# Optimization experiments

Hardware: AMD Instinct MI355X
Metric: run time of the kernel (lower is better)

Reference implementation:

```python
import jax, jax.numpy as jnp
import numpy as np

B, C, H, W = 64, 512, 8, 8
K = 100            # num_class
H1, HID, L = 64, 128, 32   # ae_hidden[0], fixed hidd, ae_latent
CLIP = 100.0       # CSSRClassifier.clip_len
RED = -0.1         # model='pcssr' -> -1, times gamma=0.1
PUSH_THRESH = 10000.0


def setup_inputs() -> dict:
    key = jax.random.key(0)
    ks = jax.random.split(key, 9)
    s = lambda fan_in: 1.0 / np.sqrt(fan_in)  # kaiming-ish 1x1 conv init scale
    return {
        "x": jax.random.normal(ks[0], (B, C, H, W), jnp.float32),
        "ycls": jax.random.randint(ks[1], (B,), 0, K),
        "safe_margin_all": jax.random.normal(ks[2], (K,), jnp.float32),
        "safe_distance_all": jax.random.normal(ks[3], (K,), jnp.float32),
        "W1": jax.random.normal(ks[4], (K, H1, C), jnp.float32) * s(C),
        "W2": jax.random.normal(ks[5], (K, HID, H1), jnp.float32) * s(H1),
        "W3": jax.random.normal(ks[6], (K, L, HID), jnp.float32) * s(HID),
        "prototypes": jax.random.normal(ks[7], (K, L, H, W), jnp.float32),
        "prototypes1": jax.random.normal(ks[8], (K, L, H, W), jnp.float32),
    }


def reference(x, ycls, safe_margin_all, safe_distance_all, W1, W2, W3, prototypes, prototypes1):
    P = H * W
    xf = x.reshape(B, C, P)
    # per-class 1x1-conv encoder (tanh after every conv), batched over classes k
    h = jnp.tanh(jnp.einsum('koc,bcp->kbop', W1, xf))      # [K,B,H1,P]
    h = jnp.tanh(jnp.einsum('koi,kbip->kbop', W2, h))      # [K,B,HID,P]
    lt = jnp.tanh(jnp.einsum('koi,kbip->kbop', W3, h))     # [K,B,L,P]
    p = prototypes.reshape(K, 1, L, P)
    p1 = prototypes1.reshape(K, 1, L, P)
    # squared-L2 distance over channel dim, scaled by reduction, clipped
    er = jnp.clip(jnp.sum((lt - p) ** 2, axis=2) * RED, -CLIP, CLIP)    # [K,B,P]
    er1 = jnp.clip(jnp.sum((lt - p1) ** 2, axis=2) * RED, -CLIP, CLIP)  # [K,B,P]
    # training losses (pull on er1, push on er), vectorized across classes
    f = jnp.sum(er, axis=2)    # [K,B] spatial-summed errors
    f1 = jnp.sum(er1, axis=2)  # [K,B]
    cls_ids = jnp.arange(K)[:, None]
    mask_eq = (ycls[None, :] == cls_ids).astype(f.dtype)   # [K,B]
    n_eq = jnp.sum(mask_eq, axis=1)
    pull = jnp.sum(jnp.where(n_eq > 0,
                             jnp.sum(f1 * mask_eq, axis=1) / jnp.maximum(n_eq, 1.0),
                             0.0))
    comb = (1.0 - mask_eq) * (f < PUSH_THRESH).astype(f.dtype)
    n_comb = jnp.sum(comb, axis=1)
    push = jnp.sum(jnp.where(n_comb > 0,
                             jnp.sum(f * comb, axis=1) / jnp.maximum(n_comb, 1.0),
                             0.0))
    # cat per-class [B,1,H,W] errors along dim 1 -> [B,K,H,W]
    logits = jnp.transpose(er, (1, 0, 2)).reshape(B, K, H, W)
    logits1 = jnp.transpose(er1, (1, 0, 2)).reshape(B, K, H, W)
    return logits, logits1, pull, push
```

## Files before the change

kernel.cpp:

```cpp
#include <hip/hip_runtime.h>

typedef short  s16x8  __attribute__((ext_vector_type(8)));
typedef float  f32x16 __attribute__((ext_vector_type(16)));
typedef unsigned short u16;
typedef unsigned int   u32;
typedef unsigned long long u64b;

#define MFMA32(a,b,c) __builtin_amdgcn_mfma_f32_32x32x16_bf16((a),(b),(c),0,0,0)
#define KCLS 100
#define VMCNT(n) asm volatile("s_waitcnt vmcnt(" #n ")" ::: "memory")
#define BAR()    __builtin_amdgcn_s_barrier()

__device__ __forceinline__ u16 f2bf(float f) {
  return (u16)(__builtin_bit_cast(unsigned, f) >> 16);
}

__device__ __forceinline__ u32 pk2bf(float lo, float hi) {
#if __has_builtin(__builtin_amdgcn_perm)
  return __builtin_amdgcn_perm(__builtin_bit_cast(u32, hi),
                               __builtin_bit_cast(u32, lo), 0x07060302u);
#else
  return (__builtin_bit_cast(u32, lo) >> 16) | (__builtin_bit_cast(u32, hi) & 0xffff0000u);
#endif
}

__device__ __forceinline__ float tanh_fast(float x) {
  float e = __builtin_amdgcn_exp2f(x * 2.8853900817779268f);
  return 1.0f - 2.0f * __builtin_amdgcn_rcpf(e + 1.0f);
}

__device__ __forceinline__ void ld_lds16(const void* g, void* l) {
  __builtin_amdgcn_global_load_lds(
      (const __attribute__((address_space(1))) unsigned char*)g,
      (__attribute__((address_space(3))) unsigned char*)l, 16, 0, 0);
}

__global__ void prep(const float* __restrict__ x, const float* __restrict__ w1,
                     const float* __restrict__ w2, const float* __restrict__ w3,
                     u16* __restrict__ xF, u16* __restrict__ W1F,
                     u16* __restrict__ W2F, u16* __restrict__ W3F,
                     float* __restrict__ fz, float* __restrict__ out2) {
  __shared__ float tile[64][65];
  const int bid = blockIdx.x, t = threadIdx.x;
  if (bid == 0 && t < 2) out2[t] = 0.f;
  if (bid < 512) {
    const int b = bid >> 3, ck = bid & 7;
    #pragma unroll
    for (int j = 0; j < 4; j++) {
      int e4 = j * 1024 + t * 4;
      int c = e4 >> 6, p0 = e4 & 63;
      float4 v = *(const float4*)(x + ((size_t)b * 512 + ck * 64 + c) * 64 + p0);
      tile[c][p0] = v.x; tile[c][p0 + 1] = v.y; tile[c][p0 + 2] = v.z; tile[c][p0 + 3] = v.w;
    }
    __syncthreads();
    #pragma unroll
    for (int i = 0; i < 2; i++) {
      int s = i * 256 + t;
      int ksl = s >> 7, ph = (s >> 6) & 1, lane = s & 63;
      int cb = ksl * 16 + (lane >> 5) * 8, pp = ph * 32 + (lane & 31);
      u16 o[8];
      #pragma unroll
      for (int jj = 0; jj < 8; jj++) o[jj] = f2bf(tile[cb + jj][pp]);
      *(uint4*)(xF + (((size_t)b * 64 + (ck * 4 + ksl) * 2 + ph) * 512) + lane * 8) = *(uint4*)o;
    }
  } else if (bid < 1312) {
    int base = (bid - 512) * 512;
    #pragma unroll
    for (int i = 0; i < 2; i++) {
      int s = base + i * 256 + t;
      int frag = s >> 6, lane = s & 63;
      int k = frag >> 6, fr = frag & 63;
      int m = (fr & 1) * 32 + (lane & 31);
      int c0 = (fr >> 1) * 16 + (lane >> 5) * 8;
      const float* src = w1 + ((size_t)k * 64 + m) * 512 + c0;
      float4 a = *(const float4*)src, b4 = *(const float4*)(src + 4);
      u16 o[8] = { f2bf(a.x), f2bf(a.y), f2bf(a.z), f2bf(a.w),
                   f2bf(b4.x), f2bf(b4.y), f2bf(b4.z), f2bf(b4.w) };
      *(uint4*)(W1F + ((size_t)frag * 512) + lane * 8) = *(uint4*)o;
    }
  } else if (bid < 1512) {
    int base = (bid - 1312) * 512;
    #pragma unroll
    for (int i = 0; i < 2; i++) {
      int s = base + i * 256 + t;
      int frag = s >> 6, lane = s & 63;
      int k = frag >> 4, fr = frag & 15;
      int m = (fr & 3) * 32 + (lane & 31);
      int c0 = (fr >> 2) * 16 + (lane >> 5) * 8;
      const float* src = w2 + ((size_t)k * 128 + m) * 64 + c0;
      float4 a = *(const float4*)src, b4 = *(const float4*)(src + 4);
      u16 o[8] = { f2bf(a.x), f2bf(a.y), f2bf(a.z), f2bf(a.w),
                   f2bf(b4.x), f2bf(b4.y), f2bf(b4.z), f2bf(b4.w) };
      *(uint4*)(W2F + ((size_t)frag * 512) + lane * 8) = *(uint4*)o;
    }
  } else if (bid < 1612) {
    int base = (bid - 1512) * 512;
    #pragma unroll
    for (int i = 0; i < 2; i++) {
      int s = base + i * 256 + t;
      int frag = s >> 6, lane = s & 63;
      int k = frag >> 3, kb = frag & 7;
      int m = lane & 31;
      int c0 = kb * 16 + (lane >> 5) * 8;
      const float* src = w3 + ((size_t)k * 32 + m) * 128 + c0;
      float4 a = *(const float4*)src, b4 = *(const float4*)(src + 4);
      u16 o[8] = { f2bf(a.x), f2bf(a.y), f2bf(a.z), f2bf(a.w),
                   f2bf(b4.x), f2bf(b4.y), f2bf(b4.z), f2bf(b4.w) };
      *(uint4*)(W3F + ((size_t)frag * 512) + lane * 8) = *(uint4*)o;
    }
  } else {
    int i4 = (bid - 1612) * 256 + t;
    if (i4 < 3200) {
      float4 z = {0.f, 0.f, 0.f, 0.f};
      *(float4*)(fz + (size_t)i4 * 4) = z;
    }
  }
}

template<int GG>
__device__ __forceinline__ s16x8 mk_bfrag(const f32x16 a) {
  u32 P0 = pk2bf(tanh_fast(a[8 * GG + 0]), tanh_fast(a[8 * GG + 1]));
  u32 P1 = pk2bf(tanh_fast(a[8 * GG + 2]), tanh_fast(a[8 * GG + 3]));
  u32 Q0 = pk2bf(tanh_fast(a[8 * GG + 4]), tanh_fast(a[8 * GG + 5]));
  u32 Q1 = pk2bf(tanh_fast(a[8 * GG + 6]), tanh_fast(a[8 * GG + 7]));
  asm("v_permlane32_swap_b32 %0, %1" : "+v"(P0), "+v"(Q0));
  asm("v_permlane32_swap_b32 %0, %1" : "+v"(P1), "+v"(Q1));
  int4 wv = { (int)P0, (int)P1, (int)Q0, (int)Q1 };
  return __builtin_bit_cast(s16x8, wv);
}

__global__ __launch_bounds__(256, 4) void cssr_main(
    const u16* __restrict__ W1F, const u16* __restrict__ W2F, const u16* __restrict__ W3F,
    const u16* __restrict__ xF, const float* __restrict__ protos,
    const float* __restrict__ protos1, float* __restrict__ out,
    float* __restrict__ fw, float* __restrict__ f1w)
{
  __shared__ u16 pool[20480];
  const int bid = blockIdx.x;
  const int k = bid >> 5, bpair = bid & 31;
  const int tid = threadIdx.x, w = tid >> 6, lane = tid & 63;
  const int bq = w >> 1, ph = w & 1;
  const int b = bpair * 2 + bq;
  const int h = lane >> 5, nn = lane & 31;

  const u16* xw  = xF  + ((size_t)b * 64) * 512 + lane * 8;
  const u16* w1w = W1F + ((size_t)k * 64) * 512 + lane * 8;

  s16x8 Bc[4], Bn[4];
  #pragma unroll
  for (int ksl = 0; ksl < 4; ksl++)
    Bc[ksl] = *(const s16x8*)(xw + (ksl * 2 + ph) * 512);
  ld_lds16(w1w + (w * 2 + 0) * 512, &pool[(2 * w + 0) * 512]);
  ld_lds16(w1w + (w * 2 + 1) * 512, &pool[(2 * w + 1) * 512]);

  f32x16 acc1[2] = {};
  #pragma unroll
  for (int ci = 0; ci < 8; ci++) {
    const int cb = ci & 1;
    if (ci < 7) {
      #pragma unroll
      for (int ksl = 0; ksl < 4; ksl++)
        Bn[ksl] = *(const s16x8*)(xw + (((ci + 1) * 4 + ksl) * 2 + ph) * 512);
      ld_lds16(w1w + (((ci + 1) * 4 + w) * 2 + 0) * 512, &pool[(cb ^ 1) * 4096 + (2 * w + 0) * 512]);
      ld_lds16(w1w + (((ci + 1) * 4 + w) * 2 + 1) * 512, &pool[(cb ^ 1) * 4096 + (2 * w + 1) * 512]);
    } else {
      #pragma unroll
      for (int j = 0; j < 4; j++)
        ld_lds16(W2F + ((size_t)k * 16 + w * 4 + j) * 512 + lane * 8,
                 &pool[8192 + (w * 4 + j) * 512]);
      ld_lds16(W3F + ((size_t)k * 8 + w * 2 + 0) * 512 + lane * 8, &pool[16384 + (w * 2 + 0) * 512]);
      ld_lds16(W3F + ((size_t)k * 8 + w * 2 + 1) * 512 + lane * 8, &pool[16384 + (w * 2 + 1) * 512]);
    }
    VMCNT(6); BAR();
    __builtin_amdgcn_s_setprio(1);
    #pragma unroll
    for (int ksl = 0; ksl < 4; ksl++) {
      s16x8 A0 = *(const s16x8*)&pool[cb * 4096 + (ksl * 2 + 0) * 512 + lane * 8];
      s16x8 A1 = *(const s16x8*)&pool[cb * 4096 + (ksl * 2 + 1) * 512 + lane * 8];
      acc1[0] = MFMA32(A0, Bc[ksl], acc1[0]);
      acc1[1] = MFMA32(A1, Bc[ksl], acc1[1]);
    }
    __builtin_amdgcn_s_setprio(0);
    if (ci < 7) {
      #pragma unroll
      for (int ksl = 0; ksl < 4; ksl++) Bc[ksl] = Bn[ksl];
      BAR();
    }
  }

  s16x8 b1[4];
  b1[0] = mk_bfrag<0>(acc1[0]); b1[1] = mk_bfrag<1>(acc1[0]);
  b1[2] = mk_bfrag<0>(acc1[1]); b1[3] = mk_bfrag<1>(acc1[1]);

  VMCNT(2); BAR();

  f32x16 acc2[4] = {};
  __builtin_amdgcn_s_setprio(1);
  #pragma unroll
  for (int kb = 0; kb < 4; kb++) {
    #pragma unroll
    for (int m4 = 0; m4 < 4; m4++) {
      s16x8 A = *(const s16x8*)&pool[8192 + (kb * 4 + m4) * 512 + lane * 8];
      acc2[m4] = MFMA32(A, b1[kb], acc2[m4]);
    }
  }
  __builtin_amdgcn_s_setprio(0);

  VMCNT(0); BAR();

  const int p = ph * 32 + nn;
  const float* pr  = protos  + (size_t)k * 2048 + p;
  const float* pr1 = protos1 + (size_t)k * 2048 + p;
  float prv[16], pr1v[16];
  #pragma unroll
  for (int g = 0; g < 4; g++) {
    #pragma unroll
    for (int q = 0; q < 4; q++) {
      int m = q + 8 * g + 4 * h;
      prv [g * 4 + q] = pr [m * 64];
      pr1v[g * 4 + q] = pr1[m * 64];
    }
  }

  s16x8 b2[8];
  b2[0] = mk_bfrag<0>(acc2[0]); b2[1] = mk_bfrag<1>(acc2[0]);
  b2[2] = mk_bfrag<0>(acc2[1]); b2[3] = mk_bfrag<1>(acc2[1]);
  b2[4] = mk_bfrag<0>(acc2[2]); b2[5] = mk_bfrag<1>(acc2[2]);
  b2[6] = mk_bfrag<0>(acc2[3]); b2[7] = mk_bfrag<1>(acc2[3]);

  f32x16 acc3 = {};
  __builtin_amdgcn_s_setprio(1);
  #pragma unroll
  for (int kb = 0; kb < 8; kb++) {
    s16x8 A = *(const s16x8*)&pool[16384 + kb * 512 + lane * 8];
    acc3 = MFMA32(A, b2[kb], acc3);
  }
  __builtin_amdgcn_s_setprio(0);

  float d2 = 0.f, d21 = 0.f;
  #pragma unroll
  for (int g = 0; g < 4; g++) {
    #pragma unroll
    for (int q = 0; q < 4; q++) {
      float lt = tanh_fast(acc3[g * 4 + q]);
      float d = lt - prv [g * 4 + q];  d2  += d * d;
      float e = lt - pr1v[g * 4 + q];  d21 += e * e;
    }
  }
  d2 += __shfl_xor(d2, 32); d21 += __shfl_xor(d21, 32);
  float er  = fminf(fmaxf(d2  * -0.1f, -100.f), 100.f);
  float er1 = fminf(fmaxf(d21 * -0.1f, -100.f), 100.f);
  if (h == 0) {
    out[(size_t)b * 6400 + k * 64 + p]          = er;
    out[409600 + (size_t)b * 6400 + k * 64 + p] = er1;
  }
  float s = er, s1 = er1;
  s += __shfl_xor(s, 1);  s1 += __shfl_xor(s1, 1);
  s += __shfl_xor(s, 2);  s1 += __shfl_xor(s1, 2);
  s += __shfl_xor(s, 4);  s1 += __shfl_xor(s1, 4);
  s += __shfl_xor(s, 8);  s1 += __shfl_xor(s1, 8);
  s += __shfl_xor(s, 16); s1 += __shfl_xor(s1, 16);
  if (lane == 0) {
    atomicAdd(&fw [k * 64 + b], s);
    atomicAdd(&f1w[k * 64 + b], s1);
  }
}

__global__ void finalize(const float* __restrict__ f, const float* __restrict__ f1,
                         const int* __restrict__ ycls, float* __restrict__ out2) {
  const int k = blockIdx.x, b = threadIdx.x;
  float fv = f[k * 64 + b], f1v = f1[k * 64 + b];
  bool eq = (ycls[b] == k);
  bool cb = (!eq) && (fv < 10000.f);
  float s1 = eq ? f1v : 0.f, ne = eq ? 1.f : 0.f;
  float s  = cb ? fv  : 0.f, nc = cb ? 1.f : 0.f;
  #pragma unroll
  for (int o = 1; o < 64; o <<= 1) {
    s1 += __shfl_xor(s1, o); ne += __shfl_xor(ne, o);
    s  += __shfl_xor(s,  o); nc += __shfl_xor(nc, o);
  }
  if (b == 0) {
    if (ne > 0.f) atomicAdd(&out2[0], s1 / ne);
    if (nc > 0.f) atomicAdd(&out2[1], s / nc);
  }
}

extern "C" void kernel_launch(void* const* d_in, const int* in_sizes, int n_in,
                              void* d_out, int out_size, void* d_ws, size_t ws_size,
                              hipStream_t stream) {
  const float* x     = (const float*)d_in[0];
  const int*   ycls  = (const int*)d_in[1];
  const float* W1    = (const float*)d_in[4];
  const float* W2    = (const float*)d_in[5];
  const float* W3    = (const float*)d_in[6];
  const float* prot  = (const float*)d_in[7];
  const float* prot1 = (const float*)d_in[8];
  float* out = (float*)d_out;

  char* ws = (char*)d_ws;
  u16*  xFb = (u16*)(ws);
  u16*  W1F = (u16*)(ws + 4194304);
  u16*  W2F = (u16*)(ws + 10747904);
  u16*  W3F = (u16*)(ws + 12386304);
  float* fw  = (float*)(ws + 13205504);
  float* f1w = (float*)(ws + 13231104);

  prep<<<1625, 256, 0, stream>>>(x, W1, W2, W3, xFb, W1F, W2F, W3F,
                                 fw, out + 819200);
  cssr_main<<<KCLS * 32, 256, 0, stream>>>(W1F, W2F, W3F, xFb, prot, prot1,
                                           out, fw, f1w);
  finalize<<<KCLS, 64, 0, stream>>>(fw, f1w, ycls, out + 819200);
}
```

Baseline: 142.0 us.

## Use four-slot LDS ring to prefetch W1 two stages ahead and stream W2/W3

Shrinks the shared pool from 20480 to 16384 u16 entries, organised as a four-slot ring. W1 chunks are prefetched two iterations ahead, which drops the second barrier in each layer-1 iteration. The W2 fragment layout is changed so each half of W2 fits one slot. Layer 2 is split into two halves and W3 is streamed into freed slots, overlapping those loads with compute and tanh packing. The smaller LDS footprint may also allow higher occupancy, but the hand-tuned vmcnt counts are fragile and easy to get wrong.

```diff
diff --git a/kernel.cpp b/kernel.cpp
--- a/kernel.cpp
+++ b/kernel.cpp
@@ -85,8 +85,8 @@
       int s = base + i * 256 + t;
       int frag = s >> 6, lane = s & 63;
       int k = frag >> 4, fr = frag & 15;
-      int m = (fr & 3) * 32 + (lane & 31);
-      int c0 = (fr >> 2) * 16 + (lane >> 5) * 8;
+      int m = (fr >> 2) * 32 + (lane & 31);
+      int c0 = (fr & 3) * 16 + (lane >> 5) * 8;
       const float* src = w2 + ((size_t)k * 128 + m) * 64 + c0;
       float4 a = *(const float4*)src, b4 = *(const float4*)(src + 4);
       u16 o[8] = { f2bf(a.x), f2bf(a.y), f2bf(a.z), f2bf(a.w),
@@ -135,7 +135,7 @@
     const float* __restrict__ protos1, float* __restrict__ out,
     float* __restrict__ fw, float* __restrict__ f1w)
 {
-  __shared__ u16 pool[20480];
+  __shared__ u16 pool[4][4096];
   const int bid = blockIdx.x;
   const int k = bid >> 5, bpair = bid & 31;
   const int tid = threadIdx.x, w = tid >> 6, lane = tid & 63;
@@ -145,68 +145,77 @@
 
   const u16* xw  = xF  + ((size_t)b * 64) * 512 + lane * 8;
   const u16* w1w = W1F + ((size_t)k * 64) * 512 + lane * 8;
-
-  s16x8 Bc[4], Bn[4];
+  const u16* w2w = W2F + ((size_t)k * 16) * 512 + lane * 8;
+  const u16* w3w = W3F + ((size_t)k * 8)  * 512 + lane * 8;
+
+  #define DMA_W1(c) { ld_lds16(w1w + ((c) * 8 + 2 * w + 0) * 512, &pool[(c) & 3][(2 * w + 0) * 512]); \
+                      ld_lds16(w1w + ((c) * 8 + 2 * w + 1) * 512, &pool[(c) & 3][(2 * w + 1) * 512]); }
+
+  s16x8 Bst[2][4];
   #pragma unroll
   for (int ksl = 0; ksl < 4; ksl++)
-    Bc[ksl] = *(const s16x8*)(xw + (ksl * 2 + ph) * 512);
-  ld_lds16(w1w + (w * 2 + 0) * 512, &pool[(2 * w + 0) * 512]);
-  ld_lds16(w1w + (w * 2 + 1) * 512, &pool[(2 * w + 1) * 512]);
+    Bst[0][ksl] = *(const s16x8*)(xw + (ksl * 2 + ph) * 512);
+  DMA_W1(0); DMA_W1(1);
 
   f32x16 acc1[2] = {};
   #pragma unroll
-  for (int ci = 0; ci < 8; ci++) {
-    const int cb = ci & 1;
-    if (ci < 7) {
-      #pragma unroll
-      for (int ksl = 0; ksl < 4; ksl++)
-        Bn[ksl] = *(const s16x8*)(xw + (((ci + 1) * 4 + ksl) * 2 + ph) * 512);
-      ld_lds16(w1w + (((ci + 1) * 4 + w) * 2 + 0) * 512, &pool[(cb ^ 1) * 4096 + (2 * w + 0) * 512]);
-      ld_lds16(w1w + (((ci + 1) * 4 + w) * 2 + 1) * 512, &pool[(cb ^ 1) * 4096 + (2 * w + 1) * 512]);
+  for (int ci = 0; ci < 7; ci++) {
+    #pragma unroll
+    for (int ksl = 0; ksl < 4; ksl++)
+      Bst[(ci + 1) & 1][ksl] = *(const s16x8*)(xw + (((ci + 1) * 4 + ksl) * 2 + ph) * 512);
+    if (ci < 6) {
+      DMA_W1(ci + 2);
     } else {
-      #pragma unroll
-      for (int j = 0; j < 4; j++)
-        ld_lds16(W2F + ((size_t)k * 16 + w * 4 + j) * 512 + lane * 8,
-                 &pool[8192 + (w * 4 + j) * 512]);
-      ld_lds16(W3F + ((size_t)k * 8 + w * 2 + 0) * 512 + lane * 8, &pool[16384 + (w * 2 + 0) * 512]);
-      ld_lds16(W3F + ((size_t)k * 8 + w * 2 + 1) * 512 + lane * 8, &pool[16384 + (w * 2 + 1) * 512]);
-    }
-    VMCNT(6); BAR();
+      ld_lds16(w2w + (2 * w + 0) * 512, &pool[0][(2 * w + 0) * 512]);
+      ld_lds16(w2w + (2 * w + 1) * 512, &pool[0][(2 * w + 1) * 512]);
+    }
+    VMCNT(8); BAR();
     __builtin_amdgcn_s_setprio(1);
     #pragma unroll
     for (int ksl = 0; ksl < 4; ksl++) {
-      s16x8 A0 = *(const s16x8*)&pool[cb * 4096 + (ksl * 2 + 0) * 512 + lane * 8];
-      s16x8 A1 = *(const s16x8*)&pool[cb * 4096 + (ksl * 2 + 1) * 512 + lane * 8];
-      acc1[0] = MFMA32(A0, Bc[ksl], acc1[0]);
-      acc1[1] = MFMA32(A1, Bc[ksl], acc1[1]);
+      s16x8 A0 = *(const s16x8*)&pool[ci & 3][(ksl * 2 + 0) * 512 + lane * 8];
+      s16x8 A1 = *(const s16x8*)&pool[ci & 3][(ksl * 2 + 1) * 512 + lane * 8];
+      acc1[0] = MFMA32(A0, Bst[ci & 1][ksl], acc1[0]);
+      acc1[1] = MFMA32(A1, Bst[ci & 1][ksl], acc1[1]);
     }
     __builtin_amdgcn_s_setprio(0);
-    if (ci < 7) {
-      #pragma unroll
-      for (int ksl = 0; ksl < 4; ksl++) Bc[ksl] = Bn[ksl];
-      BAR();
-    }
-  }
+  }
+  ld_lds16(w2w + (8 + 2 * w + 0) * 512, &pool[1][(2 * w + 0) * 512]);
+  ld_lds16(w2w + (8 + 2 * w + 1) * 512, &pool[1][(2 * w + 1) * 512]);
+  VMCNT(4); BAR();
+  __builtin_amdgcn_s_setprio(1);
+  #pragma unroll
+  for (int ksl = 0; ksl < 4; ksl++) {
+    s16x8 A0 = *(const s16x8*)&pool[3][(ksl * 2 + 0) * 512 + lane * 8];
+    s16x8 A1 = *(const s16x8*)&pool[3][(ksl * 2 + 1) * 512 + lane * 8];
+    acc1[0] = MFMA32(A0, Bst[1][ksl], acc1[0]);
+    acc1[1] = MFMA32(A1, Bst[1][ksl], acc1[1]);
+  }
+  __builtin_amdgcn_s_setprio(0);
+
+  ld_lds16(w3w + (2 * w + 0) * 512, &pool[2][(2 * w + 0) * 512]);
+  ld_lds16(w3w + (2 * w + 1) * 512, &pool[2][(2 * w + 1) * 512]);
 
   s16x8 b1[4];
   b1[0] = mk_bfrag<0>(acc1[0]); b1[1] = mk_bfrag<1>(acc1[0]);
   b1[2] = mk_bfrag<0>(acc1[1]); b1[3] = mk_bfrag<1>(acc1[1]);
 
-  VMCNT(2); BAR();
-
-  f32x16 acc2[4] = {};
-  __builtin_amdgcn_s_setprio(1);
-  #pragma unroll
-  for (int kb = 0; kb < 4; kb++) {
-    #pragma unroll
-    for (int m4 = 0; m4 < 4; m4++) {
-      s16x8 A = *(const s16x8*)&pool[8192 + (kb * 4 + m4) * 512 + lane * 8];
-      acc2[m4] = MFMA32(A, b1[kb], acc2[m4]);
-    }
-  }
-  __builtin_amdgcn_s_setprio(0);
-
-  VMCNT(0); BAR();
+  VMCNT(4); BAR();
+
+  s16x8 b2[8];
+  #pragma unroll
+  for (int m4l = 0; m4l < 2; m4l++) {
+    f32x16 a2 = {};
+    __builtin_amdgcn_s_setprio(1);
+    #pragma unroll
+    for (int kb = 0; kb < 4; kb++) {
+      s16x8 A = *(const s16x8*)&pool[0][(m4l * 4 + kb) * 512 + lane * 8];
+      a2 = MFMA32(A, b1[kb], a2);
+    }
+    __builtin_amdgcn_s_setprio(0);
+    b2[m4l * 2 + 0] = mk_bfrag<0>(a2);
+    b2[m4l * 2 + 1] = mk_bfrag<1>(a2);
+  }
 
   const int p = ph * 32 + nn;
   const float* pr  = protos  + (size_t)k * 2048 + p;
@@ -221,18 +230,29 @@
       pr1v[g * 4 + q] = pr1[m * 64];
     }
   }
-
-  s16x8 b2[8];
-  b2[0] = mk_bfrag<0>(acc2[0]); b2[1] = mk_bfrag<1>(acc2[0]);
-  b2[2] = mk_bfrag<0>(acc2[1]); b2[3] = mk_bfrag<1>(acc2[1]);
-  b2[4] = mk_bfrag<0>(acc2[2]); b2[5] = mk_bfrag<1>(acc2[2]);
-  b2[6] = mk_bfrag<0>(acc2[3]); b2[7] = mk_bfrag<1>(acc2[3]);
+  VMCNT(34); BAR();
+
+  #pragma unroll
+  for (int m4l = 0; m4l < 2; m4l++) {
+    f32x16 a2 = {};
+    __builtin_amdgcn_s_setprio(1);
+    #pragma unroll
+    for (int kb = 0; kb < 4; kb++) {
+      s16x8 A = *(const s16x8*)&pool[1][(m4l * 4 + kb) * 512 + lane * 8];
+      a2 = MFMA32(A, b1[kb], a2);
+    }
+    __builtin_amdgcn_s_setprio(0);
+    b2[4 + m4l * 2 + 0] = mk_bfrag<0>(a2);
+    b2[4 + m4l * 2 + 1] = mk_bfrag<1>(a2);
+  }
+
+  VMCNT(32); BAR();
 
   f32x16 acc3 = {};
   __builtin_amdgcn_s_setprio(1);
   #pragma unroll
   for (int kb = 0; kb < 8; kb++) {
-    s16x8 A = *(const s16x8*)&pool[16384 + kb * 512 + lane * 8];
+    s16x8 A = *(const s16x8*)&pool[2][kb * 512 + lane * 8];
     acc3 = MFMA32(A, b2[kb], acc3);
   }
   __builtin_amdgcn_s_setprio(0);
@@ -264,6 +284,7 @@
     atomicAdd(&fw [k * 64 + b], s);
     atomicAdd(&f1w[k * 64 + b], s1);
   }
+  #undef DMA_W1
 }
 
 __global__ void finalize(const float* __restrict__ f, const float* __restrict__ f1,
```

Result: no change. 141.2 us (-0.6%).
